# Optimization experiments

Measured on AMD Instinct MI355X. Metric: run time of the kernel, lower is better.

Reference implementation:

```python
import jax, jax.numpy as jnp
import numpy as np

# MoE config (matches init_kwargs): dim=512, num_experts=16, top_k=2, ffn mult=4
DIM = 512
NUM_EXPERTS = 16
TOP_K = 2
HIDDEN = 4 * DIM  # FeedForward inner dim
TOKENS = 2048
LN_EPS = 1e-5


def setup_inputs() -> dict:
    key = jax.random.key(0)
    ks = jax.random.split(key, 4)
    scaled = lambda k, shape, fan_in: (
        jax.random.normal(k, shape, dtype=jnp.float32) / np.sqrt(fan_in)
    )
    return {
        "x": jax.random.normal(ks[0], (TOKENS, DIM), dtype=jnp.float32),
        # gate: Linear(dim, num_experts, bias=False)
        "Wg": scaled(ks[1], (DIM, NUM_EXPERTS), DIM),
        # per-expert FFN params stacked on leading expert axis
        "W1": scaled(ks[2], (NUM_EXPERTS, DIM, HIDDEN), DIM),
        "b1": jnp.zeros((NUM_EXPERTS, HIDDEN), jnp.float32),
        "ln_g": jnp.ones((NUM_EXPERTS, HIDDEN), jnp.float32),
        "ln_b": jnp.zeros((NUM_EXPERTS, HIDDEN), jnp.float32),
        "W2": scaled(ks[3], (NUM_EXPERTS, HIDDEN, DIM), HIDDEN),
        "b2": jnp.zeros((NUM_EXPERTS, DIM), jnp.float32),
    }


def reference(x, Wg, W1, b1, ln_g, ln_b, W2, b2):
    # ---- routing ----
    gate_logits = x @ Wg                                   # [T, E]
    w, sel = jax.lax.top_k(gate_logits, TOP_K)             # [T, k]
    # softmax over the selected-experts axis, computed in fp32 (matches dtype=torch.float)
    w = jax.nn.softmax(w.astype(jnp.float32), axis=-1).astype(x.dtype)
    n_exp = Wg.shape[1]
    # combine[t, e] = sum_k w[t, k] * 1[sel[t, k] == e]
    combine = jnp.sum(
        w[..., None] * jax.nn.one_hot(sel, n_exp, dtype=x.dtype), axis=1
    )                                                      # [T, E]

    # ---- all experts (dense, jit-friendly dispatch) ----
    # FeedForward: Linear -> SiLU -> LayerNorm -> (Dropout=identity at eval) -> Linear
    h = jnp.einsum("td,edh->eth", x, W1) + b1[:, None, :]  # [E, T, H]
    h = jax.nn.silu(h)
    mu = jnp.mean(h, axis=-1, keepdims=True)
    var = jnp.mean(jnp.square(h - mu), axis=-1, keepdims=True)
    h = (h - mu) * jax.lax.rsqrt(var + LN_EPS)
    h = h * ln_g[:, None, :] + ln_b[:, None, :]
    y = jnp.einsum("eth,ehd->etd", h, W2) + b2[:, None, :]  # [E, T, D]

    # ---- weighted combine (scatter-add equivalent) ----
    return jnp.einsum("etd,te->td", y, combine)             # [T, D]
```

## Files before the change

### kernel.cpp

```cpp
#include <hip/hip_runtime.h>
#include <hip/hip_bf16.h>

#define TOKENS 2048
#define DIM 512
#define NEXP 16
#define HID 2048
#define CAP 320
#define NTPE (CAP / 64)
#define MTILES (NEXP * NTPE)
#define NROWS (NEXP * CAP)

typedef unsigned short ushort_t;
typedef __attribute__((ext_vector_type(8))) __bf16 bf16x8;
typedef __attribute__((ext_vector_type(4))) float f32x4;

#define OFF_CNT 0
#define OFF_LTOK 1024
#define OFF_LW 21504
#define OFF_S1 41984
#define OFF_S2 62464
#define OFF_XBF 82944
#define OFF_H 2180096
#define OFF_W1T 23151616
#define OFF_W2T 56706048

__device__ __forceinline__ ushort_t f2b(float f) {
  __bf16 b = (__bf16)f;
  return __builtin_bit_cast(unsigned short, b);
}
__device__ __forceinline__ float b2f(ushort_t u) {
  return __builtin_bit_cast(float, (unsigned)u << 16);
}

__global__ __launch_bounds__(256) void wconv_k(
    const float* __restrict__ W1, const float* __restrict__ W2,
    ushort_t* __restrict__ W1t, ushort_t* __restrict__ W2t,
    int* __restrict__ counts) {
  if (blockIdx.x == 0 && blockIdx.y == 0 && threadIdx.x < NEXP)
    counts[threadIdx.x] = 0;
  int bx = blockIdx.x;
  const float* src;
  ushort_t* dst;
  int K, N, nnc;
  if (bx < 128) { src = W1; dst = W1t; K = DIM; N = HID; nnc = 8; }
  else { src = W2; dst = W2t; K = HID; N = DIM; nnc = 2; bx -= 128; }
  int e = blockIdx.y;
  int kt = bx / nnc, nb = bx % nnc;
  int k0 = kt * 32, n0 = nb * 256;
  __shared__ ushort_t Ls[8][32 * 33];
  int t = threadIdx.x;
  int r = t >> 3, c4 = (t & 7) * 4;
  const float* sp = src + ((size_t)e * K + k0 + r) * N + n0 + c4;
  ushort_t* dp = dst + ((size_t)e * N + n0 + r) * K + k0 + c4;

  float4 v[8];
#pragma unroll
  for (int j = 0; j < 8; j++) v[j] = *(const float4*)(sp + j * 32);

#pragma unroll
  for (int j = 0; j < 8; j++) {
    Ls[j][r * 33 + c4 + 0] = f2b(v[j].x);
    Ls[j][r * 33 + c4 + 1] = f2b(v[j].y);
    Ls[j][r * 33 + c4 + 2] = f2b(v[j].z);
    Ls[j][r * 33 + c4 + 3] = f2b(v[j].w);
  }
  __syncthreads();
#pragma unroll
  for (int j = 0; j < 8; j++) {
    union { ushort_t u[4]; unsigned long long q; } o;
#pragma unroll
    for (int i = 0; i < 4; i++) o.u[i] = Ls[j][(c4 + i) * 33 + r];
    *(unsigned long long*)(dp + (size_t)(j * 32) * K) = o.q;
  }
}

__global__ __launch_bounds__(256) void router_k(
    const float* __restrict__ x, const float* __restrict__ Wg,
    ushort_t* __restrict__ xbf, int* __restrict__ counts,
    int* __restrict__ ltok, float* __restrict__ lw,
    float* __restrict__ s1, float* __restrict__ s2, float* __restrict__ out) {
  int t = threadIdx.x;
  {
    float4 z = {0.f, 0.f, 0.f, 0.f};
    float4* o4 = (float4*)out + blockIdx.x * 4096 + t;
#pragma unroll
    for (int i = 0; i < 16; i++) o4[i * 256] = z;
  }
  {
    int idx = blockIdx.x * 256 + t;
    if (idx < NROWS) { s1[idx] = 0.f; s2[idx] = 0.f; }
  }

  __shared__ float xs[4][512];
  __shared__ float lg[4][16];
  __shared__ int lcnt[NEXP];
  __shared__ int ltoks[NEXP][64];
  __shared__ float lws[NEXP][64];
  __shared__ int base_s[NEXP];

  if (t < NEXP) lcnt[t] = 0;
  __syncthreads();

  int lane = t & 63, w = t >> 6;
  int dq = lane >> 2, e4 = lane & 3;
  const float* wgp = Wg + dq * NEXP + e4 * 4;

  for (int it = 0; it < 8; it++) {
    int tok = blockIdx.x * 32 + w * 8 + it;
    const float* xr = x + (size_t)tok * DIM + lane * 8;
    float4 xa = *(const float4*)xr;
    float4 xb = *(const float4*)(xr + 4);
    union { ushort_t u[8]; uint4 v; } pk;
    pk.u[0] = f2b(xa.x); pk.u[1] = f2b(xa.y); pk.u[2] = f2b(xa.z); pk.u[3] = f2b(xa.w);
    pk.u[4] = f2b(xb.x); pk.u[5] = f2b(xb.y); pk.u[6] = f2b(xb.z); pk.u[7] = f2b(xb.w);
    *(uint4*)(xbf + (size_t)tok * DIM + lane * 8) = pk.v;
    *(float4*)&xs[w][lane * 8] = xa;
    *(float4*)&xs[w][lane * 8 + 4] = xb;

    float4 a = {0.f, 0.f, 0.f, 0.f};
#pragma unroll
    for (int kk = 0; kk < 32; kk++) {
      float xv = xs[w][kk * 16 + dq];
      float4 g = *(const float4*)(wgp + kk * 16 * NEXP);
      a.x += xv * g.x; a.y += xv * g.y; a.z += xv * g.z; a.w += xv * g.w;
    }
#pragma unroll
    for (int off = 32; off >= 4; off >>= 1) {
      a.x += __shfl_down(a.x, off);
      a.y += __shfl_down(a.y, off);
      a.z += __shfl_down(a.z, off);
      a.w += __shfl_down(a.w, off);
    }
    if (lane < 4) *(float4*)&lg[w][lane * 4] = a;
    if (lane == 0) {
      int i0 = 0;
      float v0 = lg[w][0];
#pragma unroll
      for (int e = 1; e < NEXP; e++)
        if (lg[w][e] > v0) { v0 = lg[w][e]; i0 = e; }
      int i1 = -1;
      float v1 = -3.4e38f;
#pragma unroll
      for (int e = 0; e < NEXP; e++)
        if (e != i0 && lg[w][e] > v1) { v1 = lg[w][e]; i1 = e; }
      float ex = __expf(v1 - v0);
      float w0 = 1.f / (1.f + ex);
      int p0 = atomicAdd(&lcnt[i0], 1);
      ltoks[i0][p0] = tok;
      lws[i0][p0] = w0;
      int p1 = atomicAdd(&lcnt[i1], 1);
      ltoks[i1][p1] = tok;
      lws[i1][p1] = ex / (1.f + ex);
    }
  }
  __syncthreads();
  if (t < NEXP) base_s[t] = atomicAdd(&counts[t], lcnt[t]);
  __syncthreads();
  int e = t >> 4, i0 = t & 15;
  int n = lcnt[e], b = base_s[e];
  for (int i = i0; i < n; i += 16) {
    int slot = b + i;
    if (slot < CAP) {
      ltok[e * CAP + slot] = ltoks[e][i];
      lw[e * CAP + slot] = lws[e][i];
    }
  }
}

__global__ __launch_bounds__(256) void ffn1_k(
    const ushort_t* __restrict__ W1t, const float* __restrict__ b1,
    const int* __restrict__ counts, const int* __restrict__ ltok,
    const ushort_t* __restrict__ xbf, ushort_t* __restrict__ hbuf,
    float* __restrict__ s1, float* __restrict__ s2) {
  int e = blockIdx.x / NTPE, mt = blockIdx.x % NTPE;
  int cnt = counts[e];
  if (cnt - mt * 64 <= 0) return;
  int row0 = e * CAP + mt * 64;
  int h0 = blockIdx.y * 256;

  __shared__ __align__(16) ushort_t As[2][64 * 40];

  int t = threadIdx.x;
  int lane = t & 63, wave = t >> 6;
  int quad = lane >> 4, l16 = lane & 15;

  int sr = t >> 2, sp = t & 3;
  int stok = ltok[row0 + sr];
  bool sok = (unsigned)stok < TOKENS;
  const ushort_t* sx = xbf + (size_t)(sok ? stok : 0) * DIM + sp * 8;

  int ncol = h0 + wave * 64 + l16;
  const ushort_t* bb = W1t + ((size_t)e * HID + ncol) * DIM + quad * 8;

  f32x4 acc[4][4];
#pragma unroll
  for (int a = 0; a < 4; a++)
#pragma unroll
    for (int b = 0; b < 4; b++) acc[a][b] = {0.f, 0.f, 0.f, 0.f};

  uint4 avB = {0u, 0u, 0u, 0u};
  {
    uint4 avA = {0u, 0u, 0u, 0u};
    if (sok) {
      avA = *(const uint4*)(sx);
      avB = *(const uint4*)(sx + 32);
    }
    *(uint4*)(&As[0][sr * 40 + sp * 8]) = avA;
  }
  bf16x8 bc[4];
#pragma unroll
  for (int nb = 0; nb < 4; nb++)
    bc[nb] = *(const bf16x8*)(bb + (size_t)nb * 16 * DIM);

#pragma unroll
  for (int ks = 0; ks < 16; ks++) {
    __syncthreads();
    bf16x8 bn[4];
    if (ks < 15) {
#pragma unroll
      for (int nb = 0; nb < 4; nb++)
        bn[nb] = *(const bf16x8*)(bb + (size_t)nb * 16 * DIM + (ks + 1) * 32);
    }
    uint4 avN = {0u, 0u, 0u, 0u};
    if (ks < 14 && sok) avN = *(const uint4*)(sx + (ks + 2) * 32);

    bf16x8 af[4];
#pragma unroll
    for (int mb = 0; mb < 4; mb++)
      af[mb] = *(const bf16x8*)(&As[ks & 1][(mb * 16 + l16) * 40 + quad * 8]);
#pragma unroll
    for (int mb = 0; mb < 4; mb++)
#pragma unroll
      for (int nb = 0; nb < 4; nb++)
        acc[mb][nb] = __builtin_amdgcn_mfma_f32_16x16x32_bf16(af[mb], bc[nb], acc[mb][nb], 0, 0, 0);

    if (ks < 15) {
      *(uint4*)(&As[(ks + 1) & 1][sr * 40 + sp * 8]) = avB;
      avB = avN;
#pragma unroll
      for (int nb = 0; nb < 4; nb++) bc[nb] = bn[nb];
    }
  }

  float bia[4];
#pragma unroll
  for (int nb = 0; nb < 4; nb++) bia[nb] = b1[e * HID + ncol + nb * 16];
#pragma unroll
  for (int mb = 0; mb < 4; mb++) {
#pragma unroll
    for (int i = 0; i < 4; i++) {
      int m = mb * 16 + quad * 4 + i;
      size_t rowg = (size_t)(row0 + m);
      float ps = 0.f, qs = 0.f;
#pragma unroll
      for (int nb = 0; nb < 4; nb++) {
        float v = acc[mb][nb][i] + bia[nb];
        v = v / (1.f + __expf(-v));
        hbuf[rowg * HID + ncol + nb * 16] = f2b(v);
        ps += v;
        qs += v * v;
      }
      ps += __shfl_down(ps, 8); qs += __shfl_down(qs, 8);
      ps += __shfl_down(ps, 4); qs += __shfl_down(qs, 4);
      ps += __shfl_down(ps, 2); qs += __shfl_down(qs, 2);
      ps += __shfl_down(ps, 1); qs += __shfl_down(qs, 1);
      if (l16 == 0) {
        atomicAdd(&s1[rowg], ps);
        atomicAdd(&s2[rowg], qs);
      }
    }
  }
}

__global__ __launch_bounds__(256) void ffn2_k(
    const ushort_t* __restrict__ W2t, const float* __restrict__ b2,
    const float* __restrict__ lng, const float* __restrict__ lnb,
    const int* __restrict__ counts, const int* __restrict__ ltok,
    const float* __restrict__ lw, const ushort_t* __restrict__ hbuf,
    const float* __restrict__ s1, const float* __restrict__ s2,
    float* __restrict__ out) {
  int e = blockIdx.x / NTPE, mt = blockIdx.x % NTPE;
  int cnt = counts[e];
  int valid = cnt - mt * 64;
  if (valid <= 0) return;
  valid = valid > 64 ? 64 : valid;
  int row0 = e * CAP + mt * 64;
  int n0 = blockIdx.y * 256;
  int kbeg = blockIdx.z * (HID / 2);

  __shared__ __align__(16) ushort_t As[2][64 * 40];
  __shared__ float Gs[1024];
  __shared__ float Cs[1024];

  int t = threadIdx.x;
  int lane = t & 63, wave = t >> 6;
  int quad = lane >> 4, l16 = lane & 15;

  *(float4*)&Gs[t * 4] = *(const float4*)(lng + (size_t)e * HID + kbeg + t * 4);
  *(float4*)&Cs[t * 4] = *(const float4*)(lnb + (size_t)e * HID + kbeg + t * 4);

  int sr = t >> 2, sp = t & 3;
  size_t srow = (size_t)(row0 + sr);
  const ushort_t* hr = hbuf + srow * HID + kbeg + sp * 8;
  float smu = s1[srow] * (1.f / HID);
  float var = s2[srow] * (1.f / HID) - smu * smu;
  float srs = rsqrtf(var + 1e-5f);

  int ncol = n0 + wave * 64 + l16;
  const ushort_t* bb = W2t + ((size_t)e * DIM + ncol) * HID + kbeg + quad * 8;

  f32x4 acc[4][4];
#pragma unroll
  for (int a = 0; a < 4; a++)
#pragma unroll
    for (int b = 0; b < 4; b++) acc[a][b] = {0.f, 0.f, 0.f, 0.f};

  uint4 hvA = *(const uint4*)(hr);
  uint4 hvB = *(const uint4*)(hr + 32);
  __syncthreads();

  {
    union { uint4 v; ushort_t u[8]; } hv;
    hv.v = hvA;
    int sb = sp * 8;
    union { ushort_t u[8]; uint4 v; } pk;
#pragma unroll
    for (int j = 0; j < 8; j++) {
      float f = (b2f(hv.u[j]) - smu) * srs;
      pk.u[j] = f2b(f * Gs[sb + j] + Cs[sb + j]);
    }
    *(uint4*)(&As[0][sr * 40 + sp * 8]) = pk.v;
  }
  bf16x8 bc[4];
#pragma unroll
  for (int nb = 0; nb < 4; nb++)
    bc[nb] = *(const bf16x8*)(bb + (size_t)nb * 16 * HID);

#pragma unroll 8
  for (int ks = 0; ks < 32; ks++) {
    __syncthreads();
    bf16x8 bn[4];
    if (ks < 31) {
#pragma unroll
      for (int nb = 0; nb < 4; nb++)
        bn[nb] = *(const bf16x8*)(bb + (size_t)nb * 16 * HID + (ks + 1) * 32);
    }
    uint4 hvN = {0u, 0u, 0u, 0u};
    if (ks < 30) hvN = *(const uint4*)(hr + (ks + 2) * 32);

    bf16x8 af[4];
#pragma unroll
    for (int mb = 0; mb < 4; mb++)
      af[mb] = *(const bf16x8*)(&As[ks & 1][(mb * 16 + l16) * 40 + quad * 8]);
#pragma unroll
    for (int mb = 0; mb < 4; mb++)
#pragma unroll
      for (int nb = 0; nb < 4; nb++)
        acc[mb][nb] = __builtin_amdgcn_mfma_f32_16x16x32_bf16(af[mb], bc[nb], acc[mb][nb], 0, 0, 0);

    if (ks < 31) {
      union { uint4 v; ushort_t u[8]; } hv;
      hv.v = hvB;
      int sb = (ks + 1) * 32 + sp * 8;
      union { ushort_t u[8]; uint4 v; } pk;
#pragma unroll
      for (int j = 0; j < 8; j++) {
        float f = (b2f(hv.u[j]) - smu) * srs;
        pk.u[j] = f2b(f * Gs[sb + j] + Cs[sb + j]);
      }
      *(uint4*)(&As[(ks + 1) & 1][sr * 40 + sp * 8]) = pk.v;
      hvB = hvN;
#pragma unroll
      for (int nb = 0; nb < 4; nb++) bc[nb] = bn[nb];
    }
  }

  bool addb = (blockIdx.z == 0);
  float bia[4];
#pragma unroll
  for (int nb = 0; nb < 4; nb++)
    bia[nb] = addb ? b2[e * DIM + ncol + nb * 16] : 0.f;
#pragma unroll
  for (int mb = 0; mb < 4; mb++) {
#pragma unroll
    for (int i = 0; i < 4; i++) {
      int m = mb * 16 + quad * 4 + i;
      if (m < valid) {
        int tok = ltok[row0 + m];
        float w = lw[row0 + m];
#pragma unroll
        for (int nb = 0; nb < 4; nb++) {
          float v = acc[mb][nb][i] + bia[nb];
          atomicAdd(out + (size_t)tok * DIM + ncol + nb * 16, w * v);
        }
      }
    }
  }
}

extern "C" void kernel_launch(void* const* d_in, const int* in_sizes, int n_in,
                              void* d_out, int out_size, void* d_ws, size_t ws_size,
                              hipStream_t stream) {
  const float* x = (const float*)d_in[0];
  const float* Wg = (const float*)d_in[1];
  const float* W1 = (const float*)d_in[2];
  const float* b1 = (const float*)d_in[3];
  const float* lng = (const float*)d_in[4];
  const float* lnb = (const float*)d_in[5];
  const float* W2 = (const float*)d_in[6];
  const float* b2 = (const float*)d_in[7];
  float* out = (float*)d_out;

  char* ws = (char*)d_ws;
  int* counts = (int*)(ws + OFF_CNT);
  int* ltok = (int*)(ws + OFF_LTOK);
  float* lw = (float*)(ws + OFF_LW);
  float* s1 = (float*)(ws + OFF_S1);
  float* s2 = (float*)(ws + OFF_S2);
  ushort_t* xbf = (ushort_t*)(ws + OFF_XBF);
  ushort_t* hbuf = (ushort_t*)(ws + OFF_H);
  ushort_t* W1t = (ushort_t*)(ws + OFF_W1T);
  ushort_t* W2t = (ushort_t*)(ws + OFF_W2T);

  wconv_k<<<dim3(256, NEXP), 256, 0, stream>>>(W1, W2, W1t, W2t, counts);
  router_k<<<64, 256, 0, stream>>>(x, Wg, xbf, counts, ltok, lw, s1, s2, out);
  ffn1_k<<<dim3(MTILES, HID / 256), 256, 0, stream>>>(W1t, b1, counts, ltok, xbf, hbuf, s1, s2);
  ffn2_k<<<dim3(MTILES, DIM / 256, 2), 256, 0, stream>>>(W2t, b2, lng, lnb, counts, ltok,
                                                         lw, hbuf, s1, s2, out);
}
```

Baseline: 288.7 us.

## Store converted expert weights in MFMA-tiled blocks for contiguous B-fragment loads

New measurement: 269.6 us. 6.6% less time.

```diff
diff --git a/kernel.cpp b/kernel.cpp
--- a/kernel.cpp
+++ b/kernel.cpp
@@ -47,30 +47,36 @@
   int e = blockIdx.y;
   int kt = bx / nnc, nb = bx % nnc;
   int k0 = kt * 32, n0 = nb * 256;
-  __shared__ ushort_t Ls[8][32 * 33];
+  __shared__ ushort_t Ls[32 * 264];
   int t = threadIdx.x;
   int r = t >> 3, c4 = (t & 7) * 4;
   const float* sp = src + ((size_t)e * K + k0 + r) * N + n0 + c4;
-  ushort_t* dp = dst + ((size_t)e * N + n0 + r) * K + k0 + c4;
 
   float4 v[8];
 #pragma unroll
   for (int j = 0; j < 8; j++) v[j] = *(const float4*)(sp + j * 32);
-
 #pragma unroll
   for (int j = 0; j < 8; j++) {
-    Ls[j][r * 33 + c4 + 0] = f2b(v[j].x);
-    Ls[j][r * 33 + c4 + 1] = f2b(v[j].y);
-    Ls[j][r * 33 + c4 + 2] = f2b(v[j].z);
-    Ls[j][r * 33 + c4 + 3] = f2b(v[j].w);
+    union { ushort_t u[4]; uint2 d; } p;
+    p.u[0] = f2b(v[j].x); p.u[1] = f2b(v[j].y);
+    p.u[2] = f2b(v[j].z); p.u[3] = f2b(v[j].w);
+    *(uint2*)&Ls[r * 264 + c4 + j * 32] = p.d;
   }
   __syncthreads();
-#pragma unroll
-  for (int j = 0; j < 8; j++) {
-    union { ushort_t u[4]; unsigned long long q; } o;
-#pragma unroll
-    for (int i = 0; i < 4; i++) o.u[i] = Ls[j][(c4 + i) * 33 + r];
-    *(unsigned long long*)(dp + (size_t)(j * 32) * K) = o.q;
+
+  int tile_n = t >> 4;
+  int l16 = t & 15;
+  size_t tbase =
+      ((size_t)(e * (N >> 4) + (n0 >> 4) + tile_n) * (K >> 5) + kt) * 512;
+#pragma unroll
+  for (int i = 0; i < 4; i++) {
+    int o = i * 128 + l16 * 8;
+    int nl = o >> 5, kk = o & 31;
+    int col = tile_n * 16 + nl;
+    union { ushort_t u[8]; uint4 q; } s;
+#pragma unroll
+    for (int j = 0; j < 8; j++) s.u[j] = Ls[(kk + j) * 264 + col];
+    *(uint4*)(dst + tbase + o) = s.q;
   }
 }
 
@@ -190,7 +196,8 @@
   const ushort_t* sx = xbf + (size_t)(sok ? stok : 0) * DIM + sp * 8;
 
   int ncol = h0 + wave * 64 + l16;
-  const ushort_t* bb = W1t + ((size_t)e * HID + ncol) * DIM + quad * 8;
+  const ushort_t* bb = W1t +
+      ((size_t)(e * 128 + (h0 >> 4) + wave * 4) * 16) * 512 + l16 * 32 + quad * 8;
 
   f32x4 acc[4][4];
 #pragma unroll
@@ -210,7 +217,7 @@
   bf16x8 bc[4];
 #pragma unroll
   for (int nb = 0; nb < 4; nb++)
-    bc[nb] = *(const bf16x8*)(bb + (size_t)nb * 16 * DIM);
+    bc[nb] = *(const bf16x8*)(bb + nb * 8192);
 
 #pragma unroll
   for (int ks = 0; ks < 16; ks++) {
@@ -219,7 +226,7 @@
     if (ks < 15) {
 #pragma unroll
       for (int nb = 0; nb < 4; nb++)
-        bn[nb] = *(const bf16x8*)(bb + (size_t)nb * 16 * DIM + (ks + 1) * 32);
+        bn[nb] = *(const bf16x8*)(bb + nb * 8192 + (ks + 1) * 512);
     }
     uint4 avN = {0u, 0u, 0u, 0u};
     if (ks < 14 && sok) avN = *(const uint4*)(sx + (ks + 2) * 32);
@@ -307,7 +314,9 @@
   float srs = rsqrtf(var + 1e-5f);
 
   int ncol = n0 + wave * 64 + l16;
-  const ushort_t* bb = W2t + ((size_t)e * DIM + ncol) * HID + kbeg + quad * 8;
+  const ushort_t* bb = W2t +
+      ((size_t)(e * 32 + (n0 >> 4) + wave * 4) * 64 + blockIdx.z * 32) * 512 +
+      l16 * 32 + quad * 8;
 
   f32x4 acc[4][4];
 #pragma unroll
@@ -334,7 +343,7 @@
   bf16x8 bc[4];
 #pragma unroll
   for (int nb = 0; nb < 4; nb++)
-    bc[nb] = *(const bf16x8*)(bb + (size_t)nb * 16 * HID);
+    bc[nb] = *(const bf16x8*)(bb + nb * 32768);
 
 #pragma unroll 8
   for (int ks = 0; ks < 32; ks++) {
@@ -343,7 +352,7 @@
     if (ks < 31) {
 #pragma unroll
       for (int nb = 0; nb < 4; nb++)
-        bn[nb] = *(const bf16x8*)(bb + (size_t)nb * 16 * HID + (ks + 1) * 32);
+        bn[nb] = *(const bf16x8*)(bb + nb * 32768 + (ks + 1) * 512);
     }
     uint4 hvN = {0u, 0u, 0u, 0u};
     if (ks < 30) hvN = *(const uint4*)(hr + (ks + 2) * 32);
```
